# Kernel tuning notes

Measured on AMD Instinct MI355X. Metric: run time of the kernel, lower is better.

Reference implementation:

```python
import jax, jax.numpy as jnp
import numpy as np

B = 256          # batch == num_blocks
SEQ = 128
HIDDEN = 1024
NUM_BLOCKS = 256
NUM_LABELS = 3


def setup_inputs() -> dict:
    key = jax.random.key(0)
    k1, k2, k3, k4 = jax.random.split(key, 4)
    entity_encoding = jax.random.normal(k1, (B, SEQ, HIDDEN), dtype=jnp.float32)
    states = jax.random.normal(k2, (B, NUM_BLOCKS * HIDDEN), dtype=jnp.float32)
    H_w = jax.random.normal(k3, (HIDDEN, HIDDEN), dtype=jnp.float32) * (1.0 / np.sqrt(HIDDEN))
    R_w = jax.random.normal(k4, (NUM_LABELS, HIDDEN), dtype=jnp.float32) * (1.0 / np.sqrt(HIDDEN))
    prelu_alpha = jnp.ones((HIDDEN,), dtype=jnp.float32)  # init=1.0
    return {"entity_encoding": entity_encoding, "states": states,
            "H_w": H_w, "R_w": R_w, "prelu_alpha": prelu_alpha}


def reference(entity_encoding, states, H_w, R_w, prelu_alpha):
    # x: CLS token, [B, H]
    x = entity_encoding[:, 0, :]
    # states -> [B, num_blocks, H]; chunk i of torch.chunk(..., dim=1) is S[:, i, :]
    S = states.reshape(B, NUM_BLOCKS, HIDDEN)
    # per-block dot with x, softmax over the batch axis (dim=0 in torch)
    scores = jnp.einsum('bh,bkh->bk', x, S)          # [B, nb]
    p = jax.nn.softmax(scores, axis=0)               # softmax over b
    # u[k] = sum_b p[b,k] * S[b,k,:]  -> [nb, H]; nb == B
    u = jnp.einsum('bk,bkh->kh', p, S)
    v = x + u @ H_w.T                                # [B, H]
    act = jnp.where(v >= 0, v, prelu_alpha * v)      # PReLU, per-channel alpha
    return act @ R_w.T                               # [B, num_labels]
```

## Files before the change

kernel.cpp:

```cpp
#include <hip/hip_runtime.h>
#include <math.h>

#define B_DIM 256
#define K_DIM 256
#define H_DIM 1024
#define SEQ_DIM 128
#define L_DIM 3
#define NSPLIT 4
#define BS (B_DIM / NSPLIT)
#define SK 4

__global__ void k_flash(const float* __restrict__ ent, const float* __restrict__ S,
                        float* __restrict__ num, float* __restrict__ ml) {
    int k = blockIdx.x, sp = blockIdx.y, t = threadIdx.x;
    int lane = t & 63, wave = t >> 6;
    __shared__ float red[2][4];

    float4 acc = {0.f, 0.f, 0.f, 0.f};
    float m = -INFINITY, l = 0.f;
    int b0 = sp * BS;

    const float* Sp = S   + ((size_t)(b0 * K_DIM + k)) * H_DIM + t * 4;
    const float* Xp = ent + (size_t)b0 * SEQ_DIM * H_DIM + t * 4;

    float4 s4 = *(const float4*)Sp;
    float4 x4 = *(const float4*)Xp;

    for (int bb = 0; bb < BS; ++bb) {
        float4 s4n = {0.f, 0.f, 0.f, 0.f}, x4n = {0.f, 0.f, 0.f, 0.f};
        if (bb + 1 < BS) {
            s4n = *(const float4*)(Sp + (size_t)(bb + 1) * K_DIM * H_DIM);
            x4n = *(const float4*)(Xp + (size_t)(bb + 1) * SEQ_DIM * H_DIM);
        }
        float partial = s4.x * x4.x + s4.y * x4.y + s4.z * x4.z + s4.w * x4.w;
#pragma unroll
        for (int off = 32; off > 0; off >>= 1) partial += __shfl_down(partial, off, 64);
        if (lane == 0) red[bb & 1][wave] = partial;
        __syncthreads();
        float s = red[bb & 1][0] + red[bb & 1][1] + red[bb & 1][2] + red[bb & 1][3];

        float mn = fmaxf(m, s);
        float scale = expf(m - mn);
        float e = expf(s - mn);
        acc.x = acc.x * scale + e * s4.x;
        acc.y = acc.y * scale + e * s4.y;
        acc.z = acc.z * scale + e * s4.z;
        acc.w = acc.w * scale + e * s4.w;
        l = l * scale + e;
        m = mn;

        s4 = s4n; x4 = x4n;
    }
    *(float4*)(num + ((size_t)(sp * K_DIM + k)) * H_DIM + t * 4) = acc;
    if (t == 0) {
        ml[sp * K_DIM + k] = m;
        ml[NSPLIT * K_DIM + sp * K_DIM + k] = l;
    }
}

__global__ void k_combine(const float* __restrict__ num, const float* __restrict__ ml,
                          float* __restrict__ u) {
    int k = blockIdx.x, t = threadIdx.x;
    float M = -INFINITY;
#pragma unroll
    for (int sp = 0; sp < NSPLIT; ++sp) M = fmaxf(M, ml[sp * K_DIM + k]);
    float w[NSPLIT];
    float denom = 0.f;
#pragma unroll
    for (int sp = 0; sp < NSPLIT; ++sp) {
        w[sp] = expf(ml[sp * K_DIM + k] - M);
        denom += w[sp] * ml[NSPLIT * K_DIM + sp * K_DIM + k];
    }
    float inv = 1.f / denom;
    float4 a = {0.f, 0.f, 0.f, 0.f};
#pragma unroll
    for (int sp = 0; sp < NSPLIT; ++sp) {
        float4 n4 = *(const float4*)(num + ((size_t)(sp * K_DIM + k)) * H_DIM + t * 4);
        a.x += w[sp] * n4.x; a.y += w[sp] * n4.y; a.z += w[sp] * n4.z; a.w += w[sp] * n4.w;
    }
    a.x *= inv; a.y *= inv; a.z *= inv; a.w *= inv;
    *(float4*)(u + (size_t)k * H_DIM + t * 4) = a;
}

__global__ void k_vgemm(const float* __restrict__ u, const float* __restrict__ Hw,
                        float* __restrict__ vpart) {
    __shared__ float Us[64][17];
    __shared__ float Hs[64][17];
    int tid = threadIdx.x;
    int tx = tid & 15, ty = tid >> 4;
    int hx = blockIdx.x * 64, by = blockIdx.y * 64, z = blockIdx.z;
    float acc[4][4] = {};
    int li = tid * 4;
    int r = li >> 4, cc = li & 15;
    int k0 = z * (H_DIM / SK), k1 = k0 + (H_DIM / SK);
    for (int kk0 = k0; kk0 < k1; kk0 += 16) {
        float4 uv = *(const float4*)(u  + (size_t)(by + r) * H_DIM + kk0 + cc);
        float4 hv = *(const float4*)(Hw + (size_t)(hx + r) * H_DIM + kk0 + cc);
        Us[r][cc] = uv.x; Us[r][cc + 1] = uv.y; Us[r][cc + 2] = uv.z; Us[r][cc + 3] = uv.w;
        Hs[r][cc] = hv.x; Hs[r][cc + 1] = hv.y; Hs[r][cc + 2] = hv.z; Hs[r][cc + 3] = hv.w;
        __syncthreads();
#pragma unroll
        for (int kk = 0; kk < 16; ++kk) {
            float a[4], bv[4];
#pragma unroll
            for (int i = 0; i < 4; ++i) a[i]  = Us[ty * 4 + i][kk];
#pragma unroll
            for (int j = 0; j < 4; ++j) bv[j] = Hs[tx * 4 + j][kk];
#pragma unroll
            for (int i = 0; i < 4; ++i)
#pragma unroll
                for (int j = 0; j < 4; ++j) acc[i][j] += a[i] * bv[j];
        }
        __syncthreads();
    }
#pragma unroll
    for (int i = 0; i < 4; ++i) {
        int b = by + ty * 4 + i;
#pragma unroll
        for (int j = 0; j < 4; ++j) {
            int h = hx + tx * 4 + j;
            vpart[((size_t)z * B_DIM + b) * H_DIM + h] = acc[i][j];
        }
    }
}

__global__ void k_final(const float* __restrict__ vpart, const float* __restrict__ ent,
                        const float* __restrict__ alpha, const float* __restrict__ Rw,
                        float* __restrict__ out) {
    __shared__ float sm[4 * L_DIM];
    int b = blockIdx.x, t = threadIdx.x;
    int lane = t & 63, wave = t >> 6;
    float4 v = *(const float4*)(ent + (size_t)b * SEQ_DIM * H_DIM + t * 4);
#pragma unroll
    for (int z = 0; z < SK; ++z) {
        float4 p4 = *(const float4*)(vpart + ((size_t)z * B_DIM + b) * H_DIM + t * 4);
        v.x += p4.x; v.y += p4.y; v.z += p4.z; v.w += p4.w;
    }
    float4 al = *(const float4*)(alpha + t * 4);
    v.x = (v.x >= 0.f) ? v.x : al.x * v.x;
    v.y = (v.y >= 0.f) ? v.y : al.y * v.y;
    v.z = (v.z >= 0.f) ? v.z : al.z * v.z;
    v.w = (v.w >= 0.f) ? v.w : al.w * v.w;
    float p[L_DIM];
#pragma unroll
    for (int l = 0; l < L_DIM; ++l) {
        float4 r4 = *(const float4*)(Rw + l * H_DIM + t * 4);
        p[l] = v.x * r4.x + v.y * r4.y + v.z * r4.z + v.w * r4.w;
    }
#pragma unroll
    for (int off = 32; off > 0; off >>= 1) {
#pragma unroll
        for (int l = 0; l < L_DIM; ++l) p[l] += __shfl_down(p[l], off, 64);
    }
    if (lane == 0) {
#pragma unroll
        for (int l = 0; l < L_DIM; ++l) sm[wave * L_DIM + l] = p[l];
    }
    __syncthreads();
    if (t < L_DIM) {
        out[b * L_DIM + t] = sm[t] + sm[L_DIM + t] + sm[2 * L_DIM + t] + sm[3 * L_DIM + t];
    }
}

extern "C" void kernel_launch(void* const* d_in, const int* in_sizes, int n_in,
                              void* d_out, int out_size, void* d_ws, size_t ws_size,
                              hipStream_t stream) {
    const float* ent   = (const float*)d_in[0];
    const float* S     = (const float*)d_in[1];
    const float* Hw    = (const float*)d_in[2];
    const float* Rw    = (const float*)d_in[3];
    const float* alpha = (const float*)d_in[4];
    float* out = (float*)d_out;

    float* ws    = (float*)d_ws;
    float* num   = ws;
    float* ml    = num + (size_t)NSPLIT * K_DIM * H_DIM;
    float* u     = ml + 2 * NSPLIT * K_DIM;
    float* vpart = u + (size_t)K_DIM * H_DIM;

    k_flash  <<<dim3(K_DIM, NSPLIT), 256, 0, stream>>>(ent, S, num, ml);
    k_combine<<<K_DIM, 256, 0, stream>>>(num, ml, u);
    k_vgemm  <<<dim3(H_DIM / 64, B_DIM / 64, SK), 256, 0, stream>>>(u, Hw, vpart);
    k_final  <<<B_DIM, 256, 0, stream>>>(vpart, ent, alpha, Rw, out);
}
```

Measured before the change: 441.6 us.

## Use single-wave flash blocks with xor-shuffle reduction and double split count

```diff
diff --git a/kernel.cpp b/kernel.cpp
--- a/kernel.cpp
+++ b/kernel.cpp
@@ -6,53 +6,75 @@
 #define H_DIM 1024
 #define SEQ_DIM 128
 #define L_DIM 3
-#define NSPLIT 4
+#define NSPLIT 8
 #define BS (B_DIM / NSPLIT)
 #define SK 4
 
-__global__ void k_flash(const float* __restrict__ ent, const float* __restrict__ S,
-                        float* __restrict__ num, float* __restrict__ ml) {
-    int k = blockIdx.x, sp = blockIdx.y, t = threadIdx.x;
-    int lane = t & 63, wave = t >> 6;
-    __shared__ float red[2][4];
-
-    float4 acc = {0.f, 0.f, 0.f, 0.f};
+__global__ __launch_bounds__(64) void k_flash(const float* __restrict__ ent,
+                                              const float* __restrict__ S,
+                                              float* __restrict__ num,
+                                              float* __restrict__ ml) {
+    int k = blockIdx.x, sp = blockIdx.y, lane = threadIdx.x;
+    int b0 = sp * BS;
+
+    const float* Sp = S   + ((size_t)(b0 * K_DIM + k)) * H_DIM;
+    const float* Xp = ent + (size_t)b0 * SEQ_DIM * H_DIM;
+
+    float4 acc[4] = {{0,0,0,0},{0,0,0,0},{0,0,0,0},{0,0,0,0}};
     float m = -INFINITY, l = 0.f;
-    int b0 = sp * BS;
-
-    const float* Sp = S   + ((size_t)(b0 * K_DIM + k)) * H_DIM + t * 4;
-    const float* Xp = ent + (size_t)b0 * SEQ_DIM * H_DIM + t * 4;
-
-    float4 s4 = *(const float4*)Sp;
-    float4 x4 = *(const float4*)Xp;
+
+    float4 sc[4], xc[4];
+#pragma unroll
+    for (int r = 0; r < 4; ++r) {
+        int idx = r * 256 + lane * 4;
+        sc[r] = *(const float4*)(Sp + idx);
+        xc[r] = *(const float4*)(Xp + idx);
+    }
 
     for (int bb = 0; bb < BS; ++bb) {
-        float4 s4n = {0.f, 0.f, 0.f, 0.f}, x4n = {0.f, 0.f, 0.f, 0.f};
+        float4 sn[4] = {{0,0,0,0},{0,0,0,0},{0,0,0,0},{0,0,0,0}};
+        float4 xn[4] = {{0,0,0,0},{0,0,0,0},{0,0,0,0},{0,0,0,0}};
         if (bb + 1 < BS) {
-            s4n = *(const float4*)(Sp + (size_t)(bb + 1) * K_DIM * H_DIM);
-            x4n = *(const float4*)(Xp + (size_t)(bb + 1) * SEQ_DIM * H_DIM);
-        }
-        float partial = s4.x * x4.x + s4.y * x4.y + s4.z * x4.z + s4.w * x4.w;
-#pragma unroll
-        for (int off = 32; off > 0; off >>= 1) partial += __shfl_down(partial, off, 64);
-        if (lane == 0) red[bb & 1][wave] = partial;
-        __syncthreads();
-        float s = red[bb & 1][0] + red[bb & 1][1] + red[bb & 1][2] + red[bb & 1][3];
+            const float* Snp = Sp + (size_t)(bb + 1) * K_DIM * H_DIM;
+            const float* Xnp = Xp + (size_t)(bb + 1) * SEQ_DIM * H_DIM;
+#pragma unroll
+            for (int r = 0; r < 4; ++r) {
+                int idx = r * 256 + lane * 4;
+                sn[r] = *(const float4*)(Snp + idx);
+                xn[r] = *(const float4*)(Xnp + idx);
+            }
+        }
+        float partial = 0.f;
+#pragma unroll
+        for (int r = 0; r < 4; ++r)
+            partial += sc[r].x * xc[r].x + sc[r].y * xc[r].y
+                     + sc[r].z * xc[r].z + sc[r].w * xc[r].w;
+#pragma unroll
+        for (int off = 1; off < 64; off <<= 1)
+            partial += __shfl_xor(partial, off, 64);
+        float s = partial;
 
         float mn = fmaxf(m, s);
         float scale = expf(m - mn);
         float e = expf(s - mn);
-        acc.x = acc.x * scale + e * s4.x;
-        acc.y = acc.y * scale + e * s4.y;
-        acc.z = acc.z * scale + e * s4.z;
-        acc.w = acc.w * scale + e * s4.w;
+#pragma unroll
+        for (int r = 0; r < 4; ++r) {
+            acc[r].x = acc[r].x * scale + e * sc[r].x;
+            acc[r].y = acc[r].y * scale + e * sc[r].y;
+            acc[r].z = acc[r].z * scale + e * sc[r].z;
+            acc[r].w = acc[r].w * scale + e * sc[r].w;
+        }
         l = l * scale + e;
         m = mn;
-
-        s4 = s4n; x4 = x4n;
-    }
-    *(float4*)(num + ((size_t)(sp * K_DIM + k)) * H_DIM + t * 4) = acc;
-    if (t == 0) {
+#pragma unroll
+        for (int r = 0; r < 4; ++r) { sc[r] = sn[r]; xc[r] = xn[r]; }
+    }
+
+    float* np = num + ((size_t)(sp * K_DIM + k)) * H_DIM;
+#pragma unroll
+    for (int r = 0; r < 4; ++r)
+        *(float4*)(np + r * 256 + lane * 4) = acc[r];
+    if (lane == 0) {
         ml[sp * K_DIM + k] = m;
         ml[NSPLIT * K_DIM + sp * K_DIM + k] = l;
     }
@@ -178,7 +200,7 @@
     float* u     = ml + 2 * NSPLIT * K_DIM;
     float* vpart = u + (size_t)K_DIM * H_DIM;
 
-    k_flash  <<<dim3(K_DIM, NSPLIT), 256, 0, stream>>>(ent, S, num, ml);
+    k_flash  <<<dim3(K_DIM, NSPLIT), 64, 0, stream>>>(ent, S, num, ml);
     k_combine<<<K_DIM, 256, 0, stream>>>(num, ml, u);
     k_vgemm  <<<dim3(H_DIM / 64, B_DIM / 64, SK), 256, 0, stream>>>(u, Hw, vpart);
     k_final  <<<B_DIM, 256, 0, stream>>>(vpart, ent, alpha, Rw, out);
```

New measurement: 440.4 us. No clear change (-0.3%).
